# Kernel tuning notes

Measured on AMD Instinct MI355X. Metric: run time of the kernel, lower is better.

The kernel has to match this reference:

```python
import jax, jax.numpy as jnp
import numpy as np

INPUT_DIM = 1024
HIDDEN = 256
OUT = 2
BATCH = 65536


def setup_inputs() -> dict:
    key = jax.random.key(0)
    ks = jax.random.split(key, 7)
    s_in = 1.0 / np.sqrt(INPUT_DIM)
    s_h = 1.0 / np.sqrt(HIDDEN)
    return {
        "embedding": jax.random.normal(ks[0], (BATCH, INPUT_DIM), dtype=jnp.float32),
        "ln_w": jnp.ones((INPUT_DIM,), dtype=jnp.float32),
        "ln_b": jnp.zeros((INPUT_DIM,), dtype=jnp.float32),
        "W1": jax.random.uniform(ks[1], (INPUT_DIM, HIDDEN), minval=-s_in, maxval=s_in, dtype=jnp.float32),
        "b1": jax.random.uniform(ks[2], (HIDDEN,), minval=-s_in, maxval=s_in, dtype=jnp.float32),
        "W2": jax.random.uniform(ks[3], (HIDDEN, OUT), minval=-s_h, maxval=s_h, dtype=jnp.float32),
        "b2": jax.random.uniform(ks[4], (OUT,), minval=-s_h, maxval=s_h, dtype=jnp.float32),
    }


def reference(embedding, ln_w, ln_b, W1, b1, W2, b2):
    # LayerNorm over last dim (eps=1e-5, torch default)
    mu = jnp.mean(embedding, axis=-1, keepdims=True)
    var = jnp.mean(jnp.square(embedding - mu), axis=-1, keepdims=True)
    x = (embedding - mu) * jax.lax.rsqrt(var + 1e-5) * ln_w + ln_b
    # Linear -> exact GELU (torch default) -> Linear; Dropout is a no-op (eval)
    h = jax.nn.gelu(x @ W1 + b1, approximate=False)
    return h @ W2 + b2
```

## Files before the change

### kernel.cpp

```cpp
#include <hip/hip_runtime.h>
#include <hip/hip_bf16.h>
#include <cstdint>

#define IDIM 1024
#define HID  256

typedef __attribute__((ext_vector_type(4))) float f32x4;
typedef __attribute__((ext_vector_type(8))) short short8;
typedef __attribute__((ext_vector_type(4))) unsigned int u32x4;

__device__ __forceinline__ unsigned short f2bf(float x) {
  __hip_bfloat16 h = __float2bfloat16(x);
  unsigned short r; __builtin_memcpy(&r, &h, 2); return r;
}
__device__ __forceinline__ unsigned pk_bf16(float a, float b) {
  __hip_bfloat162 h = __float22bfloat162_rn(make_float2(a, b));
  unsigned r; __builtin_memcpy(&r, &h, 4); return r;
}

__global__ __launch_bounds__(256)
void prep_kernel(const float* __restrict__ W1, const float* __restrict__ lnw,
                 const float* __restrict__ lnb, const float* __restrict__ b1,
                 unsigned short* __restrict__ w1bt, float* __restrict__ t2g,
                 float* __restrict__ tc1g) {
  const int n = blockIdx.x;
  const int t = threadIdx.x;
  const int k0 = t * 4;
  float s1 = 0.f, s2 = 0.f;
  unsigned short pk[4];
#pragma unroll
  for (int j = 0; j < 4; ++j) {
    const int k = k0 + j;
    const float v  = W1[(size_t)k * HID + n];
    const float sc = lnw[k] * v;
    s2 += sc;
    s1 = fmaf(lnb[k], v, s1);
    pk[j] = f2bf(sc);
  }
  const unsigned lo = (unsigned)pk[0] | ((unsigned)pk[1] << 16);
  const unsigned hi = (unsigned)pk[2] | ((unsigned)pk[3] << 16);
  *reinterpret_cast<uint2*>(w1bt + (size_t)n * IDIM + k0) = make_uint2(lo, hi);
#pragma unroll
  for (int d = 1; d < 64; d <<= 1) { s1 += __shfl_xor(s1, d); s2 += __shfl_xor(s2, d); }
  __shared__ float red[8];
  if ((t & 63) == 0) { red[(t >> 6) * 2] = s1; red[(t >> 6) * 2 + 1] = s2; }
  __syncthreads();
  if (t == 0) {
    tc1g[n] = red[0] + red[2] + red[4] + red[6] + b1[n];
    t2g[n]  = red[1] + red[3] + red[5] + red[7];
  }
}

__global__ __launch_bounds__(256, 2)
void head_kernel(const float* __restrict__ emb,
                 const unsigned short* __restrict__ w1bt,
                 const float* __restrict__ t2g, const float* __restrict__ tc1g,
                 const float* __restrict__ w2g, const float* __restrict__ b2g,
                 float* __restrict__ out) {
  __shared__ __align__(16) char smem[81920];
  char* const smA = smem;
  char* const smB = smem + 16384;
  float* const stats = reinterpret_cast<float*>(smem);
  float* const pout  = reinterpret_cast<float*>(smem + 512);

  const int t  = threadIdx.x;
  const int l  = t & 63;
  const int w  = t >> 6;
  const int lr = l & 15;
  const int lk = l >> 4;
  const int m0 = blockIdx.x * 64;

  const int ar  = t >> 2;
  const int acb = (t & 3) * 2;
  const float* const Ag = emb + (size_t)(m0 + ar) * IDIM + (t & 3) * 16;
  char* const aw0 = smA + ar * 128 + ((acb ^ (ar & 7)) * 16);
  char* const aw1 = smA + ar * 128 + (((acb + 1) ^ (ar & 7)) * 16);

  const int brow = w * 64 + (l >> 3);
  const int blc  = (l & 7) ^ (l >> 3);

  f32x4 acc[4][4];
#pragma unroll
  for (int i = 0; i < 4; ++i)
#pragma unroll
    for (int j = 0; j < 4; ++j) acc[i][j] = f32x4{0.f, 0.f, 0.f, 0.f};

  float sum = 0.f, ssq = 0.f;
  f32x4 fa0, fa1, fa2, fa3;

  auto issueA = [&](int s) {
    const f32x4* p = reinterpret_cast<const f32x4*>(Ag + s * 64);
    fa0 = p[0]; fa1 = p[1]; fa2 = p[2]; fa3 = p[3];
  };
  auto issueB = [&](int s, int buf) {
#pragma unroll
    for (int i = 0; i < 8; ++i) {
      char* dst = smB + buf * 32768 + (w * 8 + i) * 1024;
      const unsigned short* src =
          w1bt + (size_t)(brow + i * 8) * IDIM + s * 64 + blc * 8;
      __builtin_amdgcn_global_load_lds(
          reinterpret_cast<const __attribute__((address_space(1))) unsigned int*>(
              reinterpret_cast<uintptr_t>(src)),
          reinterpret_cast<__attribute__((address_space(3))) unsigned int*>(
              reinterpret_cast<uintptr_t>(dst)),
          16, 0, 0);
    }
  };
  auto writeA = [&](int buf) {
#pragma unroll
    for (int j = 0; j < 4; ++j) { sum += fa0[j]; ssq = fmaf(fa0[j], fa0[j], ssq); }
#pragma unroll
    for (int j = 0; j < 4; ++j) { sum += fa1[j]; ssq = fmaf(fa1[j], fa1[j], ssq); }
#pragma unroll
    for (int j = 0; j < 4; ++j) { sum += fa2[j]; ssq = fmaf(fa2[j], fa2[j], ssq); }
#pragma unroll
    for (int j = 0; j < 4; ++j) { sum += fa3[j]; ssq = fmaf(fa3[j], fa3[j], ssq); }
    const u32x4 c0 = {pk_bf16(fa0[0], fa0[1]), pk_bf16(fa0[2], fa0[3]),
                      pk_bf16(fa1[0], fa1[1]), pk_bf16(fa1[2], fa1[3])};
    const u32x4 c1 = {pk_bf16(fa2[0], fa2[1]), pk_bf16(fa2[2], fa2[3]),
                      pk_bf16(fa3[0], fa3[1]), pk_bf16(fa3[2], fa3[3])};
    *reinterpret_cast<u32x4*>(aw0 + buf * 8192) = c0;
    *reinterpret_cast<u32x4*>(aw1 + buf * 8192) = c1;
  };
  auto compute = [&](int buf) {
    const char* A = smA + buf * 8192;
    const char* B = smB + buf * 32768;
#pragma unroll
    for (int kk = 0; kk < 2; ++kk) {
      short8 av[4], bv[4];
      const int pc = ((kk * 4 + lk) ^ (lr & 7)) * 16;
#pragma unroll
      for (int mi = 0; mi < 4; ++mi)
        av[mi] = *reinterpret_cast<const short8*>(A + (mi * 16 + lr) * 128 + pc);
#pragma unroll
      for (int ni = 0; ni < 4; ++ni)
        bv[ni] = *reinterpret_cast<const short8*>(B + (w * 64 + ni * 16 + lr) * 128 + pc);
#pragma unroll
      for (int mi = 0; mi < 4; ++mi)
#pragma unroll
        for (int ni = 0; ni < 4; ++ni)
          acc[mi][ni] = __builtin_amdgcn_mfma_f32_16x16x32_bf16(av[mi], bv[ni],
                                                                acc[mi][ni], 0, 0, 0);
    }
  };

  issueA(0);
  issueB(0, 0);
  writeA(0);
  __syncthreads();

  for (int s = 0; s < 16; ++s) {
    const int c = s & 1;
    if (s < 15) { issueA(s + 1); issueB(s + 1, c ^ 1); }
    compute(c);
    if (s < 15) writeA(c ^ 1);
    __syncthreads();
  }

  sum += __shfl_xor(sum, 1); sum += __shfl_xor(sum, 2);
  ssq += __shfl_xor(ssq, 1); ssq += __shfl_xor(ssq, 2);
  if ((t & 3) == 0) {
    const float mu  = sum * (1.f / 1024.f);
    const float var = ssq * (1.f / 1024.f) - mu * mu;
    const float rs  = rsqrtf(var + 1e-5f);
    stats[ar * 2]     = mu * rs;
    stats[ar * 2 + 1] = rs;
  }
  __syncthreads();

  float po0[16], po1[16];
#pragma unroll
  for (int i = 0; i < 16; ++i) { po0[i] = 0.f; po1[i] = 0.f; }
#pragma unroll
  for (int ni = 0; ni < 4; ++ni) {
    const int n = w * 64 + ni * 16 + lr;
    const float t2n = t2g[n];
    const float tcn = tc1g[n];
    const float w20 = w2g[n * 2];
    const float w21 = w2g[n * 2 + 1];
#pragma unroll
    for (int mi = 0; mi < 4; ++mi) {
#pragma unroll
      for (int j = 0; j < 4; ++j) {
        const int r = mi * 16 + lk * 4 + j;
        const float mrs = stats[r * 2];
        const float rs  = stats[r * 2 + 1];
        const float z  = fmaf(rs, acc[mi][ni][j], fmaf(-mrs, t2n, tcn));
        const float hh = 0.5f * z * (1.f + erff(z * 0.70710678118654752f));
        po0[mi * 4 + j] = fmaf(hh, w20, po0[mi * 4 + j]);
        po1[mi * 4 + j] = fmaf(hh, w21, po1[mi * 4 + j]);
      }
    }
  }
#pragma unroll
  for (int i = 0; i < 16; ++i) {
#pragma unroll
    for (int d = 1; d < 16; d <<= 1) {
      po0[i] += __shfl_xor(po0[i], d);
      po1[i] += __shfl_xor(po1[i], d);
    }
  }
  if (lr == 0) {
#pragma unroll
    for (int mi = 0; mi < 4; ++mi)
#pragma unroll
      for (int j = 0; j < 4; ++j) {
        const int r = mi * 16 + lk * 4 + j;
        pout[(w * 64 + r) * 2 + 0] = po0[mi * 4 + j];
        pout[(w * 64 + r) * 2 + 1] = po1[mi * 4 + j];
      }
  }
  __syncthreads();
  if (t < 128) {
    const int r = t >> 1, o = t & 1;
    const float v = pout[r * 2 + o] + pout[(64 + r) * 2 + o] +
                    pout[(128 + r) * 2 + o] + pout[(192 + r) * 2 + o];
    out[(size_t)(m0 + r) * 2 + o] = v + b2g[o];
  }
}

extern "C" void kernel_launch(void* const* d_in, const int* in_sizes, int n_in,
                              void* d_out, int out_size, void* d_ws, size_t ws_size,
                              hipStream_t stream) {
  const float* emb = (const float*)d_in[0];
  const float* lnw = (const float*)d_in[1];
  const float* lnb = (const float*)d_in[2];
  const float* W1  = (const float*)d_in[3];
  const float* b1  = (const float*)d_in[4];
  const float* W2  = (const float*)d_in[5];
  const float* b2  = (const float*)d_in[6];
  float* out = (float*)d_out;

  unsigned short* w1bt = (unsigned short*)d_ws;
  float* t2g  = (float*)((char*)d_ws + 524288);
  float* tc1g = (float*)((char*)d_ws + 524288 + 1024);

  prep_kernel<<<HID, 256, 0, stream>>>(W1, lnw, lnb, b1, w1bt, t2g, tc1g);
  head_kernel<<<65536 / 64, 256, 0, stream>>>(emb, w1bt, t2g, tc1g, W2, b2, out);
}
```

Baseline: 82.95 us.

## Load W1 fragments directly from global into registers, drop LDS staging for B

The head kernel no longer stages the bf16 W1 tile in LDS through global_load_lds. Each wave now reads its B fragments straight from global memory (L2-resident) into registers, which shrinks LDS from 80KB to 16KB so more blocks can be resident per CU. The A prefetch is double-buffered in registers with a 2-step unrolled loop, and the barriers become waitcnt-lgkmcnt plus s_barrier so they do not wait on outstanding global loads. The prep kernel is also restructured so each thread handles 64 contiguous K values for one output column, with 16 columns per block. The risk is exposed global/L2 latency on B loads inside the MFMA loop, since nothing prefetches them ahead of use.

Measured after the change: 114.3 us. 37.8% more time.

```diff
diff --git a/kernel.cpp b/kernel.cpp
--- a/kernel.cpp
+++ b/kernel.cpp
@@ -9,45 +9,51 @@
 typedef __attribute__((ext_vector_type(8))) short short8;
 typedef __attribute__((ext_vector_type(4))) unsigned int u32x4;
 
-__device__ __forceinline__ unsigned short f2bf(float x) {
-  __hip_bfloat16 h = __float2bfloat16(x);
-  unsigned short r; __builtin_memcpy(&r, &h, 2); return r;
-}
 __device__ __forceinline__ unsigned pk_bf16(float a, float b) {
   __hip_bfloat162 h = __float22bfloat162_rn(make_float2(a, b));
   unsigned r; __builtin_memcpy(&r, &h, 4); return r;
 }
+
+#define LGKM_BARRIER() do { \
+  asm volatile("s_waitcnt lgkmcnt(0)" ::: "memory"); \
+  __builtin_amdgcn_s_barrier(); } while (0)
 
 __global__ __launch_bounds__(256)
 void prep_kernel(const float* __restrict__ W1, const float* __restrict__ lnw,
                  const float* __restrict__ lnb, const float* __restrict__ b1,
                  unsigned short* __restrict__ w1bt, float* __restrict__ t2g,
                  float* __restrict__ tc1g) {
-  const int n = blockIdx.x;
-  const int t = threadIdx.x;
-  const int k0 = t * 4;
+  const int t  = threadIdx.x;
+  const int ni = t & 15, kg = t >> 4;
+  const int n  = blockIdx.x * 16 + ni;
+  const int k0 = kg * 64;
   float s1 = 0.f, s2 = 0.f;
-  unsigned short pk[4];
-#pragma unroll
-  for (int j = 0; j < 4; ++j) {
+  unsigned pk[32];
+#pragma unroll
+  for (int j = 0; j < 64; j += 2) {
     const int k = k0 + j;
-    const float v  = W1[(size_t)k * HID + n];
-    const float sc = lnw[k] * v;
-    s2 += sc;
-    s1 = fmaf(lnb[k], v, s1);
-    pk[j] = f2bf(sc);
-  }
-  const unsigned lo = (unsigned)pk[0] | ((unsigned)pk[1] << 16);
-  const unsigned hi = (unsigned)pk[2] | ((unsigned)pk[3] << 16);
-  *reinterpret_cast<uint2*>(w1bt + (size_t)n * IDIM + k0) = make_uint2(lo, hi);
-#pragma unroll
-  for (int d = 1; d < 64; d <<= 1) { s1 += __shfl_xor(s1, d); s2 += __shfl_xor(s2, d); }
-  __shared__ float red[8];
-  if ((t & 63) == 0) { red[(t >> 6) * 2] = s1; red[(t >> 6) * 2 + 1] = s2; }
+    const float v0 = W1[(size_t)k * HID + n];
+    const float v1 = W1[(size_t)(k + 1) * HID + n];
+    const float sc0 = lnw[k] * v0, sc1 = lnw[k + 1] * v1;
+    s2 += sc0 + sc1;
+    s1 = fmaf(lnb[k], v0, fmaf(lnb[k + 1], v1, s1));
+    pk[j >> 1] = pk_bf16(sc0, sc1);
+  }
+  u32x4* dst = reinterpret_cast<u32x4*>(w1bt + (size_t)n * IDIM + k0);
+#pragma unroll
+  for (int i = 0; i < 8; ++i) {
+    const u32x4 v = {pk[i * 4], pk[i * 4 + 1], pk[i * 4 + 2], pk[i * 4 + 3]};
+    dst[i] = v;
+  }
+  __shared__ float red[2][16][17];
+  red[0][kg][ni] = s1; red[1][kg][ni] = s2;
   __syncthreads();
-  if (t == 0) {
-    tc1g[n] = red[0] + red[2] + red[4] + red[6] + b1[n];
-    t2g[n]  = red[1] + red[3] + red[5] + red[7];
+  if (kg == 0) {
+    float a = 0.f, b = 0.f;
+#pragma unroll
+    for (int i = 0; i < 16; ++i) { a += red[0][i][ni]; b += red[1][i][ni]; }
+    tc1g[n] = a + b1[n];
+    t2g[n]  = b;
   }
 }
 
@@ -57,9 +63,7 @@
                  const float* __restrict__ t2g, const float* __restrict__ tc1g,
                  const float* __restrict__ w2g, const float* __restrict__ b2g,
                  float* __restrict__ out) {
-  __shared__ __align__(16) char smem[81920];
-  char* const smA = smem;
-  char* const smB = smem + 16384;
+  __shared__ __align__(16) char smem[16384];
   float* const stats = reinterpret_cast<float*>(smem);
   float* const pout  = reinterpret_cast<float*>(smem + 512);
 
@@ -73,11 +77,10 @@
   const int ar  = t >> 2;
   const int acb = (t & 3) * 2;
   const float* const Ag = emb + (size_t)(m0 + ar) * IDIM + (t & 3) * 16;
-  char* const aw0 = smA + ar * 128 + ((acb ^ (ar & 7)) * 16);
-  char* const aw1 = smA + ar * 128 + (((acb + 1) ^ (ar & 7)) * 16);
-
-  const int brow = w * 64 + (l >> 3);
-  const int blc  = (l & 7) ^ (l >> 3);
+  char* const aw0 = smem + ar * 128 + ((acb ^ (ar & 7)) * 16);
+  char* const aw1 = smem + ar * 128 + (((acb + 1) ^ (ar & 7)) * 16);
+
+  const unsigned short* const bp = w1bt + (size_t)(w * 64 + lr) * IDIM + lk * 8;
 
   f32x4 acc[4][4];
 #pragma unroll
@@ -86,55 +89,39 @@
     for (int j = 0; j < 4; ++j) acc[i][j] = f32x4{0.f, 0.f, 0.f, 0.f};
 
   float sum = 0.f, ssq = 0.f;
-  f32x4 fa0, fa1, fa2, fa3;
-
-  auto issueA = [&](int s) {
-    const f32x4* p = reinterpret_cast<const f32x4*>(Ag + s * 64);
-    fa0 = p[0]; fa1 = p[1]; fa2 = p[2]; fa3 = p[3];
+
+  auto issueA = [&](int s, f32x4* S) {
+    const f32x4* p = reinterpret_cast<const f32x4*>(Ag + (size_t)s * 64);
+    S[0] = p[0]; S[1] = p[1]; S[2] = p[2]; S[3] = p[3];
   };
-  auto issueB = [&](int s, int buf) {
-#pragma unroll
-    for (int i = 0; i < 8; ++i) {
-      char* dst = smB + buf * 32768 + (w * 8 + i) * 1024;
-      const unsigned short* src =
-          w1bt + (size_t)(brow + i * 8) * IDIM + s * 64 + blc * 8;
-      __builtin_amdgcn_global_load_lds(
-          reinterpret_cast<const __attribute__((address_space(1))) unsigned int*>(
-              reinterpret_cast<uintptr_t>(src)),
-          reinterpret_cast<__attribute__((address_space(3))) unsigned int*>(
-              reinterpret_cast<uintptr_t>(dst)),
-          16, 0, 0);
-    }
-  };
-  auto writeA = [&](int buf) {
-#pragma unroll
-    for (int j = 0; j < 4; ++j) { sum += fa0[j]; ssq = fmaf(fa0[j], fa0[j], ssq); }
-#pragma unroll
-    for (int j = 0; j < 4; ++j) { sum += fa1[j]; ssq = fmaf(fa1[j], fa1[j], ssq); }
-#pragma unroll
-    for (int j = 0; j < 4; ++j) { sum += fa2[j]; ssq = fmaf(fa2[j], fa2[j], ssq); }
-#pragma unroll
-    for (int j = 0; j < 4; ++j) { sum += fa3[j]; ssq = fmaf(fa3[j], fa3[j], ssq); }
-    const u32x4 c0 = {pk_bf16(fa0[0], fa0[1]), pk_bf16(fa0[2], fa0[3]),
-                      pk_bf16(fa1[0], fa1[1]), pk_bf16(fa1[2], fa1[3])};
-    const u32x4 c1 = {pk_bf16(fa2[0], fa2[1]), pk_bf16(fa2[2], fa2[3]),
-                      pk_bf16(fa3[0], fa3[1]), pk_bf16(fa3[2], fa3[3])};
+  auto writeA = [&](f32x4* S, int buf) {
+#pragma unroll
+    for (int q = 0; q < 4; ++q)
+#pragma unroll
+      for (int j = 0; j < 4; ++j) {
+        sum += S[q][j];
+        ssq = fmaf(S[q][j], S[q][j], ssq);
+      }
+    const u32x4 c0 = {pk_bf16(S[0][0], S[0][1]), pk_bf16(S[0][2], S[0][3]),
+                      pk_bf16(S[1][0], S[1][1]), pk_bf16(S[1][2], S[1][3])};
+    const u32x4 c1 = {pk_bf16(S[2][0], S[2][1]), pk_bf16(S[2][2], S[2][3]),
+                      pk_bf16(S[3][0], S[3][1]), pk_bf16(S[3][2], S[3][3])};
     *reinterpret_cast<u32x4*>(aw0 + buf * 8192) = c0;
     *reinterpret_cast<u32x4*>(aw1 + buf * 8192) = c1;
   };
-  auto compute = [&](int buf) {
-    const char* A = smA + buf * 8192;
-    const char* B = smB + buf * 32768;
+  auto compute = [&](int s, int buf) {
+    const char* A = smem + buf * 8192;
+    const unsigned short* bs = bp + s * 64;
 #pragma unroll
     for (int kk = 0; kk < 2; ++kk) {
       short8 av[4], bv[4];
       const int pc = ((kk * 4 + lk) ^ (lr & 7)) * 16;
 #pragma unroll
+      for (int ni = 0; ni < 4; ++ni)
+        bv[ni] = *reinterpret_cast<const short8*>(bs + ni * 16 * IDIM + kk * 32);
+#pragma unroll
       for (int mi = 0; mi < 4; ++mi)
         av[mi] = *reinterpret_cast<const short8*>(A + (mi * 16 + lr) * 128 + pc);
-#pragma unroll
-      for (int ni = 0; ni < 4; ++ni)
-        bv[ni] = *reinterpret_cast<const short8*>(B + (w * 64 + ni * 16 + lr) * 128 + pc);
 #pragma unroll
       for (int mi = 0; mi < 4; ++mi)
 #pragma unroll
@@ -144,17 +131,21 @@
     }
   };
 
-  issueA(0);
-  issueB(0, 0);
-  writeA(0);
-  __syncthreads();
-
-  for (int s = 0; s < 16; ++s) {
-    const int c = s & 1;
-    if (s < 15) { issueA(s + 1); issueB(s + 1, c ^ 1); }
-    compute(c);
-    if (s < 15) writeA(c ^ 1);
-    __syncthreads();
+  f32x4 SA[4], SB[4];
+  issueA(0, SA);
+  writeA(SA, 0);
+  issueA(1, SB);
+  LGKM_BARRIER();
+
+  for (int s = 0; s < 16; s += 2) {
+    if (s + 2 < 16) issueA(s + 2, SA);
+    compute(s, 0);
+    writeA(SB, 1);
+    LGKM_BARRIER();
+    if (s + 3 < 16) issueA(s + 3, SB);
+    compute(s + 1, 1);
+    if (s + 2 < 16) writeA(SA, 0);
+    LGKM_BARRIER();
   }
 
   sum += __shfl_xor(sum, 1); sum += __shfl_xor(sum, 2);
@@ -235,6 +226,6 @@
   float* t2g  = (float*)((char*)d_ws + 524288);
   float* tc1g = (float*)((char*)d_ws + 524288 + 1024);
 
-  prep_kernel<<<HID, 256, 0, stream>>>(W1, lnw, lnb, b1, w1bt, t2g, tc1g);
+  prep_kernel<<<HID / 16, 256, 0, stream>>>(W1, lnw, lnb, b1, w1bt, t2g, tc1g);
   head_kernel<<<65536 / 64, 256, 0, stream>>>(emb, w1bt, t2g, tc1g, W2, b2, out);
 }
```
